# Kernel optimization log

Measured on AMD Instinct MI355X. Metric: run time of the kernel, lower is better.

## Reference

```python
import jax, jax.numpy as jnp
import numpy as np

B, T, D, H = 4, 2048, 512, 8
SCALE = np.float32(1.0 / np.sqrt(D))  # 'vaswani' scale, tied scalar, non-trainable
MASK_BIAS = np.float32(1e9)           # TF dense_attention masking constant


def setup_inputs() -> dict:
    key = jax.random.key(0)
    ks = jax.random.split(key, 5)
    s = 0.02  # small init so softmax logits are well-scaled
    return {
        "query": jax.random.normal(ks[0], (B, T, D), jnp.float32),
        "value": jax.random.normal(ks[1], (B, T, D), jnp.float32),
        "Wq": jax.random.normal(ks[2], (D, D * H), jnp.float32) * s,
        "bq": jnp.zeros((D * H,), jnp.float32),
        "Wk": jax.random.normal(ks[3], (D, D * H), jnp.float32) * s,
        "bk": jnp.zeros((D * H,), jnp.float32),
        "Wv": jax.random.normal(ks[4], (D, D * H), jnp.float32) * s,
        "bv": jnp.zeros((D * H,), jnp.float32),
    }


def reference(query, value, Wq, bq, Wk, bk, Wv, bv):
    # Per-head Dense projections (linear activation, depth=1): [B,T,D] -> [B,T,H*D]
    # split(axis=-1) into H heads + concat(axis=0) == reshape to [B,T,H,D]
    # (head h occupies contiguous slice [h*D:(h+1)*D] of the last axis)
    q = (query @ Wq + bq).reshape(B, T, H, D)
    k = (value @ Wk + bk).reshape(B, T, H, D)  # key defaults to value
    v = (value @ Wv + bv).reshape(B, T, H, D)
    # multiplicative scores: matmul(scale*q, k^T) -> [B,H,Tq,Tv]
    scores = jnp.einsum('bqhd,bkhd->bhqk', SCALE * q, k)
    # causal mask applied TF-style: scores -= 1e9 * (~mask)
    causal = jnp.tril(jnp.ones((T, T), bool))
    scores = jnp.where(causal, scores, scores - MASK_BIAS)
    attn = jax.nn.softmax(scores, axis=-1)          # [B,H,Tq,Tv]
    out = jnp.einsum('bhqk,bkhd->bqhd', attn, v)    # [B,Tq,H,D]
    # heads_output_mode='cat': concat heads back on feature axis
    return out.reshape(B, T, H * D)
```

## Files before the change

kernel.cpp:

```cpp
#include <hip/hip_runtime.h>
#include <stdint.h>

#define Bsz 4
#define Tsz 2048
#define Dsz 512
#define Hsz 8
#define HDsz 4096
#define Msz 8192
#define SCALE 0.044194173824159216f

typedef __attribute__((ext_vector_type(8))) short bf16x8;
typedef __attribute__((ext_vector_type(4))) float f32x4;
typedef __attribute__((ext_vector_type(4))) short s16x4;

static __device__ __forceinline__ short f2bf(float x) {
    uint32_t b = __float_as_uint(x);
    b += 0x7fff + ((b >> 16) & 1);
    return (short)(b >> 16);
}

__global__ __launch_bounds__(256) void xcast_kernel(
    const float* __restrict__ Xq, const float* __restrict__ Xv,
    short* __restrict__ Oq, short* __restrict__ Ov)
{
    int idx = blockIdx.x * 256 + threadIdx.x;
    const float* src = (idx < 1048576) ? Xq : Xv;
    short* dst = (idx < 1048576) ? Oq : Ov;
    int i = (idx < 1048576) ? idx : idx - 1048576;
    float4 v = *(const float4*)&src[(size_t)i * 4];
    s16x4 o;
    o.x = f2bf(v.x); o.y = f2bf(v.y); o.z = f2bf(v.z); o.w = f2bf(v.w);
    *(s16x4*)&dst[(size_t)i * 4] = o;
}

__global__ __launch_bounds__(256) void wtrans_kernel(
    const float* __restrict__ Wq, const float* __restrict__ Wk,
    const float* __restrict__ Wv, short* __restrict__ WtAll)
{
    const float* W = (blockIdx.z == 0) ? Wq : (blockIdx.z == 1) ? Wk : Wv;
    short* Wt = WtAll + (size_t)blockIdx.z * (size_t)HDsz * Dsz;
    __shared__ float tile[32][33];
    int tx = threadIdx.x, ty = threadIdx.y;
    int k0 = blockIdx.x * 32, n0 = blockIdx.y * 32;
    for (int i = 0; i < 4; i++)
        tile[ty + i * 8][tx] = W[(size_t)(k0 + ty + i * 8) * HDsz + n0 + tx];
    __syncthreads();
    for (int i = 0; i < 4; i++)
        Wt[(size_t)(n0 + ty + i * 8) * Dsz + k0 + tx] = f2bf(tile[tx][ty + i * 8]);
}

__global__ __launch_bounds__(256, 3) void proj_gemm_kernel(
    const short* __restrict__ Xqb, const short* __restrict__ Xvb,
    const short* __restrict__ WtAll, const float* __restrict__ bq,
    const float* __restrict__ bk, const float* __restrict__ bv,
    short* __restrict__ Qo, short* __restrict__ Ko, short* __restrict__ Vto)
{
    const int mode = blockIdx.z;
    const short* X = (mode == 0) ? Xqb : Xvb;
    const short* Wt = WtAll + (size_t)mode * (size_t)HDsz * Dsz;
    const float* bias = (mode == 0) ? bq : (mode == 1) ? bk : bv;
    const int m0 = blockIdx.x * 128, n0 = blockIdx.y * 128;

    __shared__ short sm[17408];

    const int tid = threadIdx.x;
    const int lane = tid & 63, wave = tid >> 6;
    const int quad = lane >> 4, l16 = lane & 15;
    const int wm = wave >> 1, wn = wave & 1;

    const int dmarow = lane >> 2;
    const int dmachunk = (lane & 3) ^ ((lane >> 3) & 3);
    const int rdsw = (quad ^ ((l16 >> 1) & 3)) * 8;

    f32x4 acc[4][4];
    for (int i = 0; i < 4; i++)
        for (int j = 0; j < 4; j++)
            acc[i][j] = f32x4{0.f, 0.f, 0.f, 0.f};

#define STAGE(ksv, bufsel) do {                                                  \
        const int _ks = (ksv);                                                   \
        short* _A = sm + (bufsel) * 4096;                                        \
        short* _B = sm + 8192 + (bufsel) * 4096;                                 \
        for (int s = 0; s < 2; s++) {                                            \
            int c = wave * 2 + s;                                                \
            int row = c * 16 + dmarow;                                           \
            const short* ga = X + (size_t)(m0 + row) * Dsz + _ks + dmachunk * 8; \
            __builtin_amdgcn_global_load_lds(                                    \
                (const __attribute__((address_space(1))) void*)ga,               \
                (__attribute__((address_space(3))) void*)&_A[c * 512], 16, 0, 0);\
            const short* gb = Wt + (size_t)(n0 + row) * Dsz + _ks + dmachunk * 8;\
            __builtin_amdgcn_global_load_lds(                                    \
                (const __attribute__((address_space(1))) void*)gb,               \
                (__attribute__((address_space(3))) void*)&_B[c * 512], 16, 0, 0);\
        }                                                                        \
    } while (0)

    STAGE(0, 0);
    __syncthreads();

    for (int t = 0; t < 16; t++) {
        const int cur = t & 1;
        if (t < 15) STAGE((t + 1) * 32, cur ^ 1);
        const short* Ac = sm + cur * 4096;
        const short* Bc = sm + 8192 + cur * 4096;
        bf16x8 af[4], bfr[4];
        for (int i = 0; i < 4; i++)
            af[i] = *(const bf16x8*)&Ac[(wm * 64 + i * 16 + l16) * 32 + rdsw];
        for (int j = 0; j < 4; j++)
            bfr[j] = *(const bf16x8*)&Bc[(wn * 64 + j * 16 + l16) * 32 + rdsw];
        for (int i = 0; i < 4; i++)
            for (int j = 0; j < 4; j++)
                acc[i][j] = __builtin_amdgcn_mfma_f32_16x16x32_bf16(
                    af[i], bfr[j], acc[i][j], 0, 0, 0);
        __syncthreads();
    }
#undef STAGE

    const int b = m0 >> 11, t0 = m0 & 2047;
    const int h = n0 >> 9, d0 = n0 & 511;
    const float scv = (mode == 0) ? SCALE : 1.0f;

    if (mode == 2) {
        for (int i = 0; i < 4; i++)
            for (int j = 0; j < 4; j++) {
                int c = wn * 64 + j * 16 + l16;
                float bb = bias[n0 + c];
                int rb = wm * 64 + i * 16 + quad * 4;
                for (int r = 0; r < 4; r++)
                    sm[c * 136 + rb + r] = f2bf(acc[i][j][r] + bb);
            }
    } else {
        for (int i = 0; i < 4; i++)
            for (int j = 0; j < 4; j++) {
                int c = wn * 64 + j * 16 + l16;
                float bb = bias[n0 + c];
                int rb = wm * 64 + i * 16 + quad * 4;
                for (int r = 0; r < 4; r++)
                    sm[(rb + r) * 136 + c] = f2bf((acc[i][j][r] + bb) * scv);
            }
    }
    __syncthreads();

    if (mode == 2) {
        size_t base = ((size_t)(b * Hsz + h) * Dsz + d0) * Tsz + t0;
        for (int k = 0; k < 8; k++) {
            int cid = k * 256 + tid;
            int c = cid >> 4, r8 = (cid & 15) * 8;
            *(bf16x8*)&Vto[base + (size_t)c * Tsz + r8] =
                *(const bf16x8*)&sm[c * 136 + r8];
        }
    } else {
        short* O = (mode == 0) ? Qo : Ko;
        size_t base = ((size_t)(b * Hsz + h) * Tsz + t0) * Dsz + d0;
        for (int k = 0; k < 8; k++) {
            int cid = k * 256 + tid;
            int r = cid >> 4, c8 = (cid & 15) * 8;
            *(bf16x8*)&O[base + (size_t)r * Dsz + c8] =
                *(const bf16x8*)&sm[r * 136 + c8];
        }
    }
}

__global__ __launch_bounds__(512, 2) void attn_kernel(
    const short* __restrict__ Q, const short* __restrict__ K,
    const short* __restrict__ Vt, float* __restrict__ out)
{
    extern __shared__ short smem[];

    const int bid = blockIdx.x;
    const int qt = 15 - (bid >> 5);
    const int bh = bid & 31;
    const int q0 = qt * 128;
    const short* Qb = Q + (size_t)bh * Tsz * Dsz;
    const short* Kb = K + (size_t)bh * Tsz * Dsz;
    const short* Vb = Vt + (size_t)bh * Dsz * Tsz;

    const int tid = threadIdx.x;
    const int lane = tid & 63, wave = tid >> 6;
    const int quad = lane >> 4, l16 = lane & 15;
    const int qw = q0 + wave * 16;
    short* Pw = smem + 74240 + wave * 640;
    const int vrow = tid >> 2, vch = tid & 3;

    bf16x8 qf[16];
    for (int ks = 0; ks < 16; ks++)
        qf[ks] = *(const bf16x8*)&Qb[(size_t)(qw + l16) * Dsz + ks * 32 + quad * 8];

    f32x4 acc[32];
    for (int i = 0; i < 32; i++) acc[i] = f32x4{0.f, 0.f, 0.f, 0.f};
    float lacc[4] = {0.f, 0.f, 0.f, 0.f};

    {
        short* Ks0 = smem;
        short* Vs0 = smem + 33280;
        for (int i = 0; i < 4; i++) {
            int r = wave * 4 + i;
            const short* gp = Kb + (size_t)r * Dsz + lane * 8;
            __builtin_amdgcn_global_load_lds(
                (const __attribute__((address_space(1))) void*)gp,
                (__attribute__((address_space(3))) void*)&Ks0[r * 520], 16, 0, 0);
        }
        for (int p = 0; p < 4; p++) {
            int row = p * 128 + vrow;
            bf16x8 v = *(const bf16x8*)&Vb[(size_t)row * Tsz + vch * 8];
            *(bf16x8*)&Vs0[row * 40 + vch * 8] = v;
        }
    }
    __syncthreads();

    const int nkv = 4 * (qt + 1);
    for (int kt = 0; kt < nkv; kt++) {
        const int kv0 = kt * 32;
        short* Ksc = smem + (kt & 1) * 16640;
        short* Vsc = smem + 33280 + (kt & 1) * 20480;
        const bool pref = (kt + 1 < nkv);

        bf16x8 vreg[4];
        if (pref) {
            const int kvn = kv0 + 32;
            short* Ksn = smem + ((kt + 1) & 1) * 16640;
            for (int i = 0; i < 4; i++) {
                int r = wave * 4 + i;
                const short* gp = Kb + (size_t)(kvn + r) * Dsz + lane * 8;
                __builtin_amdgcn_global_load_lds(
                    (const __attribute__((address_space(1))) void*)gp,
                    (__attribute__((address_space(3))) void*)&Ksn[r * 520], 16, 0, 0);
            }
            for (int p = 0; p < 4; p++) {
                int row = p * 128 + vrow;
                vreg[p] = *(const bf16x8*)&Vb[(size_t)row * Tsz + kvn + vch * 8];
            }
        }

        if (kv0 <= qw + 15) {
            f32x4 s0 = f32x4{0.f, 0.f, 0.f, 0.f}, s1 = f32x4{0.f, 0.f, 0.f, 0.f};
            for (int ks = 0; ks < 16; ks++) {
                bf16x8 b0 = *(const bf16x8*)&Ksc[l16 * 520 + ks * 32 + quad * 8];
                bf16x8 b1 = *(const bf16x8*)&Ksc[(16 + l16) * 520 + ks * 32 + quad * 8];
                s0 = __builtin_amdgcn_mfma_f32_16x16x32_bf16(qf[ks], b0, s0, 0, 0, 0);
                s1 = __builtin_amdgcn_mfma_f32_16x16x32_bf16(qf[ks], b1, s1, 0, 0, 0);
            }
            bool full = (kv0 + 31 <= qw);
            for (int r = 0; r < 4; r++) {
                int rowg = qw + quad * 4 + r;
                float p0 = __expf(fminf(s0[r], 40.f));
                float p1 = __expf(fminf(s1[r], 40.f));
                if (!full) {
                    if (kv0 + l16 > rowg) p0 = 0.f;
                    if (kv0 + 16 + l16 > rowg) p1 = 0.f;
                }
                lacc[r] += p0 + p1;
                Pw[(quad * 4 + r) * 40 + l16] = f2bf(p0);
                Pw[(quad * 4 + r) * 40 + 16 + l16] = f2bf(p1);
            }
        }
        __syncthreads();

        {
            bf16x8 vb[4];
            for (int df = 0; df < 4; df++)
                vb[df] = *(const bf16x8*)&Vsc[(wave * 64 + df * 16 + l16) * 40 + quad * 8];
            for (int rf = 0; rf < 8; rf++) {
                if (kv0 <= q0 + rf * 16 + 15) {
                    bf16x8 pa = *(const bf16x8*)&smem[74240 + rf * 640 + l16 * 40 + quad * 8];
                    for (int df = 0; df < 4; df++)
                        acc[rf * 4 + df] = __builtin_amdgcn_mfma_f32_16x16x32_bf16(
                            pa, vb[df], acc[rf * 4 + df], 0, 0, 0);
                }
            }
        }

        if (pref) {
            short* Vsn = smem + 33280 + ((kt + 1) & 1) * 20480;
            for (int p = 0; p < 4; p++) {
                int row = p * 128 + vrow;
                *(bf16x8*)&Vsn[row * 40 + vch * 8] = vreg[p];
            }
        }
        __syncthreads();
    }

    float* lsh = (float*)(smem + 74240);
    for (int r = 0; r < 4; r++) {
        float l = lacc[r];
        l += __shfl_xor(l, 1);
        l += __shfl_xor(l, 2);
        l += __shfl_xor(l, 4);
        l += __shfl_xor(l, 8);
        if (l16 == 0) lsh[wave * 16 + quad * 4 + r] = l;
    }
    __syncthreads();

    const int b = bh >> 3, h = bh & 7;
    for (int rf = 0; rf < 8; rf++) {
        for (int r = 0; r < 4; r++) {
            float invl = 1.0f / lsh[rf * 16 + quad * 4 + r];
            int t = q0 + rf * 16 + quad * 4 + r;
            float* op = &out[(size_t)(b * Tsz + t) * HDsz + h * Dsz + wave * 64 + l16];
            for (int df = 0; df < 4; df++)
                op[df * 16] = acc[rf * 4 + df][r] * invl;
        }
    }
}

extern "C" void kernel_launch(void* const* d_in, const int* in_sizes, int n_in,
                              void* d_out, int out_size, void* d_ws, size_t ws_size,
                              hipStream_t stream) {
    const float* query = (const float*)d_in[0];
    const float* value = (const float*)d_in[1];
    const float* Wq = (const float*)d_in[2];
    const float* bq = (const float*)d_in[3];
    const float* Wk = (const float*)d_in[4];
    const float* bk = (const float*)d_in[5];
    const float* Wv = (const float*)d_in[6];
    const float* bv = (const float*)d_in[7];
    float* out = (float*)d_out;

    char* ws = (char*)d_ws;
    short* Wt  = (short*)ws;
    short* Xqb = (short*)(ws + 12582912);
    short* Xvb = (short*)(ws + 20971520);
    short* Qb  = (short*)(ws + 29360128);
    short* Kb  = (short*)(ws + 96468992);
    short* Vtb = (short*)(ws + 163577856);

    (void)hipFuncSetAttribute((const void*)attn_kernel,
                        hipFuncAttributeMaxDynamicSharedMemorySize, 158720);

    xcast_kernel<<<8192, 256, 0, stream>>>(query, value, Xqb, Xvb);
    wtrans_kernel<<<dim3(16, 128, 3), dim3(32, 8), 0, stream>>>(Wq, Wk, Wv, Wt);
    proj_gemm_kernel<<<dim3(64, 32, 3), 256, 0, stream>>>(
        Xqb, Xvb, Wt, bq, bk, bv, Qb, Kb, Vtb);
    attn_kernel<<<dim3(512), dim3(512), 158720, stream>>>(Qb, Kb, Vtb, out);
}
```

Measured before the change: 547.1 us.

## Pair causal query tiles per block, swizzle K/V LDS layout, double-buffer P

The attention kernel now launches 256 blocks, and each block handles two query tiles (ib and 15-ib) in sequence, so every block does a balanced amount of causal work. The K and V shared-memory tiles switch from padded strides to XOR-swizzled unpadded layouts to avoid bank conflicts. The P buffer is double-buffered, which removes one barrier per KV step, and the V store for the next tile now happens before the PV MFMA. The projection GEMM's launch bound drops from 3 to 2 waves per SIMD, which allows more registers but lowers occupancy.

```diff
diff --git a/kernel.cpp b/kernel.cpp
--- a/kernel.cpp
+++ b/kernel.cpp
@@ -49,7 +49,7 @@
         Wt[(size_t)(n0 + ty + i * 8) * Dsz + k0 + tx] = f2bf(tile[tx][ty + i * 8]);
 }
 
-__global__ __launch_bounds__(256, 3) void proj_gemm_kernel(
+__global__ __launch_bounds__(256, 2) void proj_gemm_kernel(
     const short* __restrict__ Xqb, const short* __restrict__ Xvb,
     const short* __restrict__ WtAll, const float* __restrict__ bq,
     const float* __restrict__ bk, const float* __restrict__ bv,
@@ -167,10 +167,9 @@
 {
     extern __shared__ short smem[];
 
-    const int bid = blockIdx.x;
-    const int qt = 15 - (bid >> 5);
-    const int bh = bid & 31;
-    const int q0 = qt * 128;
+    const int idx = blockIdx.x;
+    const int bh = (idx & 7) * 4 + ((idx >> 3) & 3);
+    const int ib = idx >> 5;
     const short* Qb = Q + (size_t)bh * Tsz * Dsz;
     const short* Kb = K + (size_t)bh * Tsz * Dsz;
     const short* Vb = Vt + (size_t)bh * Dsz * Tsz;
@@ -178,127 +177,153 @@
     const int tid = threadIdx.x;
     const int lane = tid & 63, wave = tid >> 6;
     const int quad = lane >> 4, l16 = lane & 15;
-    const int qw = q0 + wave * 16;
-    short* Pw = smem + 74240 + wave * 640;
+    const int kswz = (l16 >> 1) & 7;
+    const int vrsw = (l16 >> 1) & 3;
     const int vrow = tid >> 2, vch = tid & 3;
-
-    bf16x8 qf[16];
-    for (int ks = 0; ks < 16; ks++)
-        qf[ks] = *(const bf16x8*)&Qb[(size_t)(qw + l16) * Dsz + ks * 32 + quad * 8];
-
-    f32x4 acc[32];
-    for (int i = 0; i < 32; i++) acc[i] = f32x4{0.f, 0.f, 0.f, 0.f};
-    float lacc[4] = {0.f, 0.f, 0.f, 0.f};
-
-    {
-        short* Ks0 = smem;
-        short* Vs0 = smem + 33280;
-        for (int i = 0; i < 4; i++) {
-            int r = wave * 4 + i;
-            const short* gp = Kb + (size_t)r * Dsz + lane * 8;
-            __builtin_amdgcn_global_load_lds(
-                (const __attribute__((address_space(1))) void*)gp,
-                (__attribute__((address_space(3))) void*)&Ks0[r * 520], 16, 0, 0);
-        }
-        for (int p = 0; p < 4; p++) {
-            int row = p * 128 + vrow;
-            bf16x8 v = *(const bf16x8*)&Vb[(size_t)row * Tsz + vch * 8];
-            *(bf16x8*)&Vs0[row * 40 + vch * 8] = v;
-        }
-    }
-    __syncthreads();
-
-    const int nkv = 4 * (qt + 1);
-    for (int kt = 0; kt < nkv; kt++) {
-        const int kv0 = kt * 32;
-        short* Ksc = smem + (kt & 1) * 16640;
-        short* Vsc = smem + 33280 + (kt & 1) * 20480;
-        const bool pref = (kt + 1 < nkv);
-
-        bf16x8 vreg[4];
-        if (pref) {
-            const int kvn = kv0 + 32;
-            short* Ksn = smem + ((kt + 1) & 1) * 16640;
+    const int cswz = (vrow >> 1) & 3;
+    const int b = bh >> 3, h = bh & 7;
+
+    for (int pass = 0; pass < 2; pass++) {
+        const int qt = (pass == 0) ? ib : 15 - ib;
+        const int q0 = qt * 128;
+        const int qw = q0 + wave * 16;
+
+        bf16x8 qf[16];
+#pragma unroll
+        for (int ks = 0; ks < 16; ks++)
+            qf[ks] = *(const bf16x8*)&Qb[(size_t)(qw + l16) * Dsz + ks * 32 + quad * 8];
+
+        f32x4 acc[32];
+#pragma unroll
+        for (int i = 0; i < 32; i++) acc[i] = f32x4{0.f, 0.f, 0.f, 0.f};
+        float lacc[4] = {0.f, 0.f, 0.f, 0.f};
+
+        {
+#pragma unroll
             for (int i = 0; i < 4; i++) {
                 int r = wave * 4 + i;
-                const short* gp = Kb + (size_t)(kvn + r) * Dsz + lane * 8;
+                const short* gp = Kb + (size_t)r * Dsz + (lane ^ ((r >> 1) & 7)) * 8;
                 __builtin_amdgcn_global_load_lds(
                     (const __attribute__((address_space(1))) void*)gp,
-                    (__attribute__((address_space(3))) void*)&Ksn[r * 520], 16, 0, 0);
-            }
+                    (__attribute__((address_space(3))) void*)&smem[r * 512], 16, 0, 0);
+            }
+#pragma unroll
             for (int p = 0; p < 4; p++) {
                 int row = p * 128 + vrow;
-                vreg[p] = *(const bf16x8*)&Vb[(size_t)row * Tsz + kvn + vch * 8];
-            }
-        }
-
-        if (kv0 <= qw + 15) {
-            f32x4 s0 = f32x4{0.f, 0.f, 0.f, 0.f}, s1 = f32x4{0.f, 0.f, 0.f, 0.f};
-            for (int ks = 0; ks < 16; ks++) {
-                bf16x8 b0 = *(const bf16x8*)&Ksc[l16 * 520 + ks * 32 + quad * 8];
-                bf16x8 b1 = *(const bf16x8*)&Ksc[(16 + l16) * 520 + ks * 32 + quad * 8];
-                s0 = __builtin_amdgcn_mfma_f32_16x16x32_bf16(qf[ks], b0, s0, 0, 0, 0);
-                s1 = __builtin_amdgcn_mfma_f32_16x16x32_bf16(qf[ks], b1, s1, 0, 0, 0);
-            }
-            bool full = (kv0 + 31 <= qw);
+                bf16x8 v = *(const bf16x8*)&Vb[(size_t)row * Tsz + vch * 8];
+                *(bf16x8*)&smem[32768 + row * 32 + (vch ^ cswz) * 8] = v;
+            }
+        }
+        __syncthreads();
+
+        const int nkv = 4 * (qt + 1);
+        for (int kt = 0; kt < nkv; kt++) {
+            const int kv0 = kt * 32;
+            const short* Ksc = smem + (kt & 1) * 16384;
+            short* Pc = smem + 65536 + (kt & 1) * 5120;
+            const bool pref = (kt + 1 < nkv);
+
+            bf16x8 vreg[4];
+            if (pref) {
+                const int kvn = kv0 + 32;
+                short* Ksn = smem + ((kt + 1) & 1) * 16384;
+#pragma unroll
+                for (int i = 0; i < 4; i++) {
+                    int r = wave * 4 + i;
+                    const short* gp = Kb + (size_t)(kvn + r) * Dsz
+                                    + (lane ^ ((r >> 1) & 7)) * 8;
+                    __builtin_amdgcn_global_load_lds(
+                        (const __attribute__((address_space(1))) void*)gp,
+                        (__attribute__((address_space(3))) void*)&Ksn[r * 512], 16, 0, 0);
+                }
+#pragma unroll
+                for (int p = 0; p < 4; p++) {
+                    int row = p * 128 + vrow;
+                    vreg[p] = *(const bf16x8*)&Vb[(size_t)row * Tsz + kvn + vch * 8];
+                }
+            }
+
+            if (kv0 <= qw + 15) {
+                f32x4 s0 = f32x4{0.f, 0.f, 0.f, 0.f}, s1 = f32x4{0.f, 0.f, 0.f, 0.f};
+#pragma unroll
+                for (int ks = 0; ks < 16; ks++) {
+                    int c = ((ks * 4 + quad) ^ kswz) * 8;
+                    bf16x8 b0 = *(const bf16x8*)&Ksc[l16 * 512 + c];
+                    bf16x8 b1 = *(const bf16x8*)&Ksc[(16 + l16) * 512 + c];
+                    s0 = __builtin_amdgcn_mfma_f32_16x16x32_bf16(qf[ks], b0, s0, 0, 0, 0);
+                    s1 = __builtin_amdgcn_mfma_f32_16x16x32_bf16(qf[ks], b1, s1, 0, 0, 0);
+                }
+                bool full = (kv0 + 31 <= qw);
+                short* Pw = Pc + wave * 640;
+#pragma unroll
+                for (int r = 0; r < 4; r++) {
+                    int rowg = qw + quad * 4 + r;
+                    float p0 = __expf(fminf(s0[r], 40.f));
+                    float p1 = __expf(fminf(s1[r], 40.f));
+                    if (!full) {
+                        if (kv0 + l16 > rowg) p0 = 0.f;
+                        if (kv0 + 16 + l16 > rowg) p1 = 0.f;
+                    }
+                    lacc[r] += p0 + p1;
+                    Pw[(quad * 4 + r) * 40 + l16] = f2bf(p0);
+                    Pw[(quad * 4 + r) * 40 + 16 + l16] = f2bf(p1);
+                }
+            }
+            __syncthreads();
+
+            if (pref) {
+                short* Vsn = smem + 32768 + ((kt + 1) & 1) * 16384;
+#pragma unroll
+                for (int p = 0; p < 4; p++) {
+                    int row = p * 128 + vrow;
+                    *(bf16x8*)&Vsn[row * 32 + (vch ^ cswz) * 8] = vreg[p];
+                }
+            }
+
+            {
+                const short* Vsc = smem + 32768 + (kt & 1) * 16384;
+                bf16x8 vb[4];
+#pragma unroll
+                for (int df = 0; df < 4; df++)
+                    vb[df] = *(const bf16x8*)
+                        &Vsc[(wave * 64 + df * 16 + l16) * 32 + (quad ^ vrsw) * 8];
+#pragma unroll
+                for (int rf = 0; rf < 8; rf++) {
+                    if (kv0 <= q0 + rf * 16 + 15) {
+                        bf16x8 pa = *(const bf16x8*)&Pc[rf * 640 + l16 * 40 + quad * 8];
+#pragma unroll
+                        for (int df = 0; df < 4; df++)
+                            acc[rf * 4 + df] = __builtin_amdgcn_mfma_f32_16x16x32_bf16(
+                                pa, vb[df], acc[rf * 4 + df], 0, 0, 0);
+                    }
+                }
+            }
+        }
+
+        float* lsh = (float*)(smem + 75776);
+#pragma unroll
+        for (int r = 0; r < 4; r++) {
+            float l = lacc[r];
+            l += __shfl_xor(l, 1);
+            l += __shfl_xor(l, 2);
+            l += __shfl_xor(l, 4);
+            l += __shfl_xor(l, 8);
+            if (l16 == 0) lsh[wave * 16 + quad * 4 + r] = l;
+        }
+        __syncthreads();
+
+#pragma unroll
+        for (int rf = 0; rf < 8; rf++) {
+#pragma unroll
             for (int r = 0; r < 4; r++) {
-                int rowg = qw + quad * 4 + r;
-                float p0 = __expf(fminf(s0[r], 40.f));
-                float p1 = __expf(fminf(s1[r], 40.f));
-                if (!full) {
-                    if (kv0 + l16 > rowg) p0 = 0.f;
-                    if (kv0 + 16 + l16 > rowg) p1 = 0.f;
-                }
-                lacc[r] += p0 + p1;
-                Pw[(quad * 4 + r) * 40 + l16] = f2bf(p0);
-                Pw[(quad * 4 + r) * 40 + 16 + l16] = f2bf(p1);
-            }
-        }
-        __syncthreads();
-
-        {
-            bf16x8 vb[4];
-            for (int df = 0; df < 4; df++)
-                vb[df] = *(const bf16x8*)&Vsc[(wave * 64 + df * 16 + l16) * 40 + quad * 8];
-            for (int rf = 0; rf < 8; rf++) {
-                if (kv0 <= q0 + rf * 16 + 15) {
-                    bf16x8 pa = *(const bf16x8*)&smem[74240 + rf * 640 + l16 * 40 + quad * 8];
-                    for (int df = 0; df < 4; df++)
-                        acc[rf * 4 + df] = __builtin_amdgcn_mfma_f32_16x16x32_bf16(
-                            pa, vb[df], acc[rf * 4 + df], 0, 0, 0);
-                }
-            }
-        }
-
-        if (pref) {
-            short* Vsn = smem + 33280 + ((kt + 1) & 1) * 20480;
-            for (int p = 0; p < 4; p++) {
-                int row = p * 128 + vrow;
-                *(bf16x8*)&Vsn[row * 40 + vch * 8] = vreg[p];
-            }
-        }
-        __syncthreads();
-    }
-
-    float* lsh = (float*)(smem + 74240);
-    for (int r = 0; r < 4; r++) {
-        float l = lacc[r];
-        l += __shfl_xor(l, 1);
-        l += __shfl_xor(l, 2);
-        l += __shfl_xor(l, 4);
-        l += __shfl_xor(l, 8);
-        if (l16 == 0) lsh[wave * 16 + quad * 4 + r] = l;
-    }
-    __syncthreads();
-
-    const int b = bh >> 3, h = bh & 7;
-    for (int rf = 0; rf < 8; rf++) {
-        for (int r = 0; r < 4; r++) {
-            float invl = 1.0f / lsh[rf * 16 + quad * 4 + r];
-            int t = q0 + rf * 16 + quad * 4 + r;
-            float* op = &out[(size_t)(b * Tsz + t) * HDsz + h * Dsz + wave * 64 + l16];
-            for (int df = 0; df < 4; df++)
-                op[df * 16] = acc[rf * 4 + df][r] * invl;
+                float invl = 1.0f / lsh[rf * 16 + quad * 4 + r];
+                int t = q0 + rf * 16 + quad * 4 + r;
+                float* op = &out[(size_t)(b * Tsz + t) * HDsz + h * Dsz
+                                 + wave * 64 + l16];
+#pragma unroll
+                for (int df = 0; df < 4; df++)
+                    op[df * 16] = acc[rf * 4 + df][r] * invl;
+            }
         }
     }
 }
@@ -325,11 +350,11 @@
     short* Vtb = (short*)(ws + 163577856);
 
     (void)hipFuncSetAttribute((const void*)attn_kernel,
-                        hipFuncAttributeMaxDynamicSharedMemorySize, 158720);
+                        hipFuncAttributeMaxDynamicSharedMemorySize, 152064);
 
     xcast_kernel<<<8192, 256, 0, stream>>>(query, value, Xqb, Xvb);
     wtrans_kernel<<<dim3(16, 128, 3), dim3(32, 8), 0, stream>>>(Wq, Wk, Wv, Wt);
     proj_gemm_kernel<<<dim3(64, 32, 3), 256, 0, stream>>>(
         Xqb, Xvb, Wt, bq, bk, bv, Qb, Kb, Vtb);
-    attn_kernel<<<dim3(512), dim3(512), 158720, stream>>>(Qb, Kb, Vtb, out);
-}
+    attn_kernel<<<dim3(256), dim3(512), 152064, stream>>>(Qb, Kb, Vtb, out);
+}
```

New measurement: 762.6 us. 39.4% more time.
